# Performance work log

Hardware: AMD Instinct MI355X
Metric: run time of the kernel (lower is better)

Reference implementation:

```python
import jax, jax.numpy as jnp
import numpy as np

N_NODES = 262144
N_EDGES = 4194304
NUM_GRAPHS = 1024
K = 2          # k clusters / particles
D = 4          # particle_latent_dim
D_Q = D // 2   # position part of latent


def setup_inputs() -> dict:
    key = jax.random.key(0)
    ks = jax.random.split(key, 20)
    w = lambda i, shape: 0.1 * jax.random.normal(ks[i], shape, jnp.float32)
    return {
        "x": jax.random.normal(ks[0], (N_NODES, 4), jnp.float32),
        "pos": jax.random.normal(ks[1], (N_NODES, 3), jnp.float32),
        "edge_index": jax.random.randint(ks[2], (2, N_EDGES), 0, N_NODES),
        "batch": jnp.sort(jax.random.randint(ks[3], (N_NODES,), 0, NUM_GRAPHS)),
        "enc_w1": w(4, (9, 16)), "enc_b1": jnp.zeros((16,), jnp.float32),
        "enc_w2": w(5, (16, 16)), "enc_b2": jnp.zeros((16,), jnp.float32),
        "pool_w": w(6, (16, K)), "pool_b": jnp.zeros((K,), jnp.float32),
        "toz_w": w(7, (16, D)), "toz_b": jnp.zeros((D,), jnp.float32),
        "vp_w1": w(8, (1, 32)), "vp_b1": jnp.zeros((32,), jnp.float32),
        "vp_w2": w(9, (32, 1)), "vp_b2": jnp.zeros((1,), jnp.float32),
        "bridge_w": w(10, (K * D, 8 * 4)), "bridge_b": jnp.zeros((8 * 4,), jnp.float32),
    }


def reference(x, pos, edge_index, batch,
              enc_w1, enc_b1, enc_w2, enc_b2,
              pool_w, pool_b, toz_w, toz_b,
              vp_w1, vp_b1, vp_w2, vp_b2,
              bridge_w, bridge_b):
    src = edge_index[0]  # j (source)
    dst = edge_index[1]  # i (target, PyG default flow)

    # --- EquiLayer: edge gather -> small MLP message -> mean scatter ---
    rel_pos = pos[src] - pos[dst]
    dist = jnp.linalg.norm(rel_pos, axis=-1, keepdims=True)       # [E,1]
    feat = jnp.concatenate([x[dst], x[src], dist], axis=-1)       # [E,9]
    msg = jax.nn.silu(feat @ enc_w1 + enc_b1) @ enc_w2 + enc_b2   # [E,16]
    agg = jax.ops.segment_sum(msg, dst, num_segments=N_NODES)     # [N,16]
    cnt = jax.ops.segment_sum(jnp.ones((msg.shape[0], 1), msg.dtype), dst,
                              num_segments=N_NODES)
    h = jax.nn.relu(agg / jnp.maximum(cnt, 1.0))                  # [N,16]

    # --- softmax-weighted scatter pooling over graphs ---
    s = jax.nn.softmax(h @ pool_w + pool_b, axis=-1)              # [N,K]
    weighted = s[:, :, None] * h[:, None, :]                      # [N,K,16]
    pooled = jax.ops.segment_sum(weighted, batch, num_segments=NUM_GRAPHS)  # [B,K,16]
    z = pooled @ toz_w + toz_b                                    # [B,K,D]

    # --- decode ---
    recon = (z.reshape(z.shape[0], -1) @ bridge_w + bridge_b).reshape(-1, 8, 4)

    # --- pairwise potential + forces on position part of latent ---
    iu0, iu1 = np.triu_indices(K, 1)

    def potential(q):
        diff = q[:, :, None, :] - q[:, None, :, :]
        d = jnp.sqrt(jnp.sum(diff * diff, axis=-1) + 1e-6)        # [B,K,K]
        d_flat = d[:, iu0, iu1][..., None]                        # [B,P,1]
        v = jax.nn.softplus(d_flat @ vp_w1 + vp_b1) @ vp_w2 + vp_b2
        return v.sum(axis=1)                                      # [B,1]

    q = z[..., :D_Q]
    V = potential(q)
    forces = -jax.grad(lambda qq: potential(qq).sum())(q)
    return recon, z, s, forces, V
```

## Files before the change

kernel.cpp:

```cpp
#include <hip/hip_runtime.h>
#include <math.h>

#define N_NODES   262144
#define N_EDGES   4194304
#define NUM_GRAPHS 1024
#define NBKT      256
#define BNODE     1024
#define CAPK      17408
#define EPB       8192
#define CSTRIDE   32

typedef _Float16 h8 __attribute__((ext_vector_type(8)));

static __device__ __forceinline__ float fast_rcp(float v) {
    return __builtin_amdgcn_rcpf(v);
}

__global__ __launch_bounds__(512) void bin_pack_kernel(
    const int* __restrict__ ei, const float* __restrict__ x,
    const float* __restrict__ pos,
    int* __restrict__ cursor, int* __restrict__ staged,
    h8* __restrict__ xp)
{
    __shared__ int cnt[NBKT], rcnt[NBKT], lbase[NBKT], gbase[NBKT];
    __shared__ int stage[EPB];
    __shared__ int wsum[4];
    int tid = threadIdx.x;
    if (tid < NBKT) { cnt[tid] = 0; rcnt[tid] = 0; }
    __syncthreads();

    {
        int n0 = blockIdx.x * 512 + tid;
        float4 xv0 = *(const float4*)(x + 4*n0);
        h8 o0;
        o0[0] = (_Float16)xv0.x; o0[1] = (_Float16)xv0.y;
        o0[2] = (_Float16)xv0.z; o0[3] = (_Float16)xv0.w;
        o0[4] = (_Float16)pos[3*n0+0]; o0[5] = (_Float16)pos[3*n0+1];
        o0[6] = (_Float16)pos[3*n0+2]; o0[7] = (_Float16)0.0f;
        xp[n0] = o0;
    }

    int base = blockIdx.x * EPB;
    const int4* d4 = (const int4*)(ei + N_EDGES + base);
    const int4* s4 = (const int4*)(ei + base);
    int4 dv[4];
    #pragma unroll
    for (int i = 0; i < 4; ++i) {
        dv[i] = d4[i*512 + tid];
        atomicAdd(&cnt[dv[i].x >> 10], 1);
        atomicAdd(&cnt[dv[i].y >> 10], 1);
        atomicAdd(&cnt[dv[i].z >> 10], 1);
        atomicAdd(&cnt[dv[i].w >> 10], 1);
    }
    __syncthreads();

    int lane = tid & 63, wid = tid >> 6;
    if (tid < NBKT) {
        int c = cnt[tid];
        int inc = c;
        #pragma unroll
        for (int o = 1; o < 64; o <<= 1) {
            int t = __shfl_up(inc, o);
            if (lane >= o) inc += t;
        }
        if (lane == 63) wsum[wid] = inc;
        cnt[tid] = inc;
    }
    __syncthreads();
    if (tid < NBKT) {
        int inc = cnt[tid];
        int c   = inc;
        int wb = 0;
        #pragma unroll
        for (int w = 0; w < 4; ++w) if (w < wid) wb += wsum[w];
        int prev = __shfl_up(inc, 1);
        int excl = (lane == 0) ? 0 : prev;
        lbase[tid] = wb + excl;
        c = inc - excl;
        gbase[tid] = c ? atomicAdd(cursor + tid*CSTRIDE, c) : 0;
        rcnt[tid] = 0;
    }
    __syncthreads();

    #pragma unroll
    for (int i = 0; i < 4; ++i) {
        int4 sv = s4[i*512 + tid];
        int d, s, bk, r;
        d = dv[i].x; s = sv.x; bk = d >> 10; r = atomicAdd(&rcnt[bk], 1);
        stage[lbase[bk] + r] = ((d & 1023) << 18) | s;
        d = dv[i].y; s = sv.y; bk = d >> 10; r = atomicAdd(&rcnt[bk], 1);
        stage[lbase[bk] + r] = ((d & 1023) << 18) | s;
        d = dv[i].z; s = sv.z; bk = d >> 10; r = atomicAdd(&rcnt[bk], 1);
        stage[lbase[bk] + r] = ((d & 1023) << 18) | s;
        d = dv[i].w; s = sv.w; bk = d >> 10; r = atomicAdd(&rcnt[bk], 1);
        stage[lbase[bk] + r] = ((d & 1023) << 18) | s;
    }
    __syncthreads();

    int sub = tid & 31;
    int grp = tid >> 5;
    #pragma unroll
    for (int pass = 0; pass < NBKT/16; ++pass) {
        int bk  = pass*16 + grp;
        int c2  = rcnt[bk];
        int lb  = lbase[bk];
        int gb  = gbase[bk];
        int lim = CAPK - gb; if (c2 > lim) c2 = lim;
        for (int k = sub; k < c2; k += 32)
            staged[bk*CAPK + gb + k] = stage[lb + k];
    }
}

static __device__ __forceinline__ void edge_contrib(
    const float* __restrict__ sw1, const float* __restrict__ hd,
    float4 xs, float dist, float* __restrict__ acc)
{
    float h[16];
    #pragma unroll
    for (int j4 = 0; j4 < 4; ++j4) {
        float4 w = *(const float4*)&sw1[4*16 + 4*j4];
        h[4*j4+0] = fmaf(xs.x, w.x, hd[4*j4+0]);
        h[4*j4+1] = fmaf(xs.x, w.y, hd[4*j4+1]);
        h[4*j4+2] = fmaf(xs.x, w.z, hd[4*j4+2]);
        h[4*j4+3] = fmaf(xs.x, w.w, hd[4*j4+3]);
    }
    #pragma unroll
    for (int j4 = 0; j4 < 4; ++j4) {
        float4 w = *(const float4*)&sw1[5*16 + 4*j4];
        h[4*j4+0] = fmaf(xs.y, w.x, h[4*j4+0]);
        h[4*j4+1] = fmaf(xs.y, w.y, h[4*j4+1]);
        h[4*j4+2] = fmaf(xs.y, w.z, h[4*j4+2]);
        h[4*j4+3] = fmaf(xs.y, w.w, h[4*j4+3]);
    }
    #pragma unroll
    for (int j4 = 0; j4 < 4; ++j4) {
        float4 w = *(const float4*)&sw1[6*16 + 4*j4];
        h[4*j4+0] = fmaf(xs.z, w.x, h[4*j4+0]);
        h[4*j4+1] = fmaf(xs.z, w.y, h[4*j4+1]);
        h[4*j4+2] = fmaf(xs.z, w.z, h[4*j4+2]);
        h[4*j4+3] = fmaf(xs.z, w.w, h[4*j4+3]);
    }
    #pragma unroll
    for (int j4 = 0; j4 < 4; ++j4) {
        float4 w = *(const float4*)&sw1[7*16 + 4*j4];
        h[4*j4+0] = fmaf(xs.w, w.x, h[4*j4+0]);
        h[4*j4+1] = fmaf(xs.w, w.y, h[4*j4+1]);
        h[4*j4+2] = fmaf(xs.w, w.z, h[4*j4+2]);
        h[4*j4+3] = fmaf(xs.w, w.w, h[4*j4+3]);
    }
    #pragma unroll
    for (int j4 = 0; j4 < 4; ++j4) {
        float4 w = *(const float4*)&sw1[8*16 + 4*j4];
        h[4*j4+0] = fmaf(dist, w.x, h[4*j4+0]);
        h[4*j4+1] = fmaf(dist, w.y, h[4*j4+1]);
        h[4*j4+2] = fmaf(dist, w.z, h[4*j4+2]);
        h[4*j4+3] = fmaf(dist, w.w, h[4*j4+3]);
    }
    #pragma unroll
    for (int j = 0; j < 16; ++j) {
        float sg = fast_rcp(1.0f + __expf(-h[j]));
        acc[j] = fmaf(h[j], sg, acc[j]);
    }
}

__global__ __launch_bounds__(1024, 4) void fused_node_kernel(
    const h8* __restrict__ xp,
    const int* __restrict__ cursor, const int* __restrict__ staged,
    const int* __restrict__ batch,
    const float* __restrict__ w1, const float* __restrict__ b1,
    const float* __restrict__ w2, const float* __restrict__ b2,
    const float* __restrict__ pw, const float* __restrict__ pb,
    float* __restrict__ s_out, float* __restrict__ pooled)
{
    __shared__ int esrc[CAPK];
    __shared__ int ldeg[BNODE];
    __shared__ int wsum[16];
    __shared__ __align__(16) float sw1[144];
    __shared__ float sb1[16];
    __shared__ __align__(16) float sw2[256];
    __shared__ float sb2[16];
    __shared__ float spw[32];
    __shared__ float spb[2];

    int tid = threadIdx.x;
    if (tid < 144) sw1[tid] = w1[tid];
    if (tid >= 144 && tid < 160) sb1[tid - 144] = b1[tid - 144];
    if (tid >= 160 && tid < 176) sb2[tid - 160] = b2[tid - 160];
    if (tid >= 176 && tid < 208) spw[tid - 176] = pw[tid - 176];
    if (tid >= 208 && tid < 210) spb[tid - 208] = pb[tid - 208];
    if (tid >= 256 && tid < 512) sw2[tid - 256] = w2[tid - 256];
    ldeg[tid] = 0;
    __syncthreads();

    int bkt  = blockIdx.x;
    int cnt  = cursor[bkt*CSTRIDE]; if (cnt > CAPK) cnt = CAPK;
    int base = bkt * CAPK;
    int nb0  = bkt * BNODE;

    for (int i = tid; i < cnt; i += 1024)
        atomicAdd(&ldeg[__builtin_nontemporal_load(&staged[base + i]) >> 18], 1);
    __syncthreads();

    int dg   = ldeg[tid];
    int lane = tid & 63, wid = tid >> 6;
    int inc  = dg;
    #pragma unroll
    for (int o = 1; o < 64; o <<= 1) {
        int t = __shfl_up(inc, o);
        if (lane >= o) inc += t;
    }
    if (lane == 63) wsum[wid] = inc;
    __syncthreads();
    int wb = 0;
    #pragma unroll
    for (int w = 0; w < 16; ++w) if (w < wid) wb += wsum[w];
    int r0 = wb + inc - dg;
    ldeg[tid] = r0;
    __syncthreads();

    for (int i = tid; i < cnt; i += 1024) {
        int p  = __builtin_nontemporal_load(&staged[base + i]);
        int lo = p >> 18;
        int r  = atomicAdd(&ldeg[lo], 1);
        esrc[r] = p & 0x3FFFF;
    }
    __syncthreads();

    int n = nb0 + tid;
    h8 rd = xp[n];
    float4 xd = make_float4((float)rd[0], (float)rd[1], (float)rd[2], (float)rd[3]);
    float pdx = (float)rd[4], pdy = (float)rd[5], pdz = (float)rd[6];

    float hd[16];
    #pragma unroll
    for (int j = 0; j < 16; ++j) hd[j] = sb1[j];
    #pragma unroll
    for (int j4 = 0; j4 < 4; ++j4) {
        float4 w0 = *(const float4*)&sw1[0*16 + 4*j4];
        float4 w1r = *(const float4*)&sw1[1*16 + 4*j4];
        float4 w2r = *(const float4*)&sw1[2*16 + 4*j4];
        float4 w3r = *(const float4*)&sw1[3*16 + 4*j4];
        hd[4*j4+0] = fmaf(xd.x, w0.x, hd[4*j4+0]);
        hd[4*j4+1] = fmaf(xd.x, w0.y, hd[4*j4+1]);
        hd[4*j4+2] = fmaf(xd.x, w0.z, hd[4*j4+2]);
        hd[4*j4+3] = fmaf(xd.x, w0.w, hd[4*j4+3]);
        hd[4*j4+0] = fmaf(xd.y, w1r.x, hd[4*j4+0]);
        hd[4*j4+1] = fmaf(xd.y, w1r.y, hd[4*j4+1]);
        hd[4*j4+2] = fmaf(xd.y, w1r.z, hd[4*j4+2]);
        hd[4*j4+3] = fmaf(xd.y, w1r.w, hd[4*j4+3]);
        hd[4*j4+0] = fmaf(xd.z, w2r.x, hd[4*j4+0]);
        hd[4*j4+1] = fmaf(xd.z, w2r.y, hd[4*j4+1]);
        hd[4*j4+2] = fmaf(xd.z, w2r.z, hd[4*j4+2]);
        hd[4*j4+3] = fmaf(xd.z, w2r.w, hd[4*j4+3]);
        hd[4*j4+0] = fmaf(xd.w, w3r.x, hd[4*j4+0]);
        hd[4*j4+1] = fmaf(xd.w, w3r.y, hd[4*j4+1]);
        hd[4*j4+2] = fmaf(xd.w, w3r.z, hd[4*j4+2]);
        hd[4*j4+3] = fmaf(xd.w, w3r.w, hd[4*j4+3]);
    }

    float acc[16];
    #pragma unroll
    for (int j = 0; j < 16; ++j) acc[j] = 0.0f;

    int k = 0;
    for (; k + 2 <= dg; k += 2) {
        int s0 = esrc[r0 + k];
        int s1 = esrc[r0 + k + 1];
        h8 e0 = xp[s0];
        h8 e1 = xp[s1];

        float4 a0 = make_float4((float)e0[0], (float)e0[1], (float)e0[2], (float)e0[3]);
        float dx0 = (float)e0[4] - pdx, dy0 = (float)e0[5] - pdy, dz0 = (float)e0[6] - pdz;
        float dist0 = sqrtf(fmaf(dx0, dx0, fmaf(dy0, dy0, dz0*dz0)));
        edge_contrib(sw1, hd, a0, dist0, acc);

        float4 a1 = make_float4((float)e1[0], (float)e1[1], (float)e1[2], (float)e1[3]);
        float dx1 = (float)e1[4] - pdx, dy1 = (float)e1[5] - pdy, dz1 = (float)e1[6] - pdz;
        float dist1 = sqrtf(fmaf(dx1, dx1, fmaf(dy1, dy1, dz1*dz1)));
        edge_contrib(sw1, hd, a1, dist1, acc);
    }
    if (k < dg) {
        int s0 = esrc[r0 + k];
        h8 e0 = xp[s0];
        float4 a0 = make_float4((float)e0[0], (float)e0[1], (float)e0[2], (float)e0[3]);
        float dx0 = (float)e0[4] - pdx, dy0 = (float)e0[5] - pdy, dz0 = (float)e0[6] - pdz;
        float dist0 = sqrtf(fmaf(dx0, dx0, fmaf(dy0, dy0, dz0*dz0)));
        edge_contrib(sw1, hd, a0, dist0, acc);
    }

    float c = (float)dg;
    float inv = fast_rcp(fmaxf(c, 1.0f));
    float h[16];
    #pragma unroll
    for (int j = 0; j < 16; ++j) h[j] = c * sb2[j];
    #pragma unroll
    for (int i = 0; i < 16; ++i) {
        float f = acc[i];
        #pragma unroll
        for (int j4 = 0; j4 < 4; ++j4) {
            float4 w = *(const float4*)&sw2[i*16 + 4*j4];
            h[4*j4+0] = fmaf(f, w.x, h[4*j4+0]);
            h[4*j4+1] = fmaf(f, w.y, h[4*j4+1]);
            h[4*j4+2] = fmaf(f, w.z, h[4*j4+2]);
            h[4*j4+3] = fmaf(f, w.w, h[4*j4+3]);
        }
    }
    #pragma unroll
    for (int j = 0; j < 16; ++j) h[j] = fmaxf(h[j] * inv, 0.0f);

    float l0 = spb[0], l1 = spb[1];
    #pragma unroll
    for (int j = 0; j < 16; ++j) {
        l0 = fmaf(h[j], spw[2*j+0], l0);
        l1 = fmaf(h[j], spw[2*j+1], l1);
    }
    float m = fmaxf(l0, l1);
    float e0 = __expf(l0 - m), e1 = __expf(l1 - m);
    float r = fast_rcp(e0 + e1);
    float s0 = e0 * r, s1 = e1 * r;
    s_out[2*n+0] = s0;
    s_out[2*n+1] = s1;

    float w[32];
    #pragma unroll
    for (int j = 0; j < 16; ++j) { w[j] = s0 * h[j]; w[16+j] = s1 * h[j]; }

    int b = batch[n];
    #pragma unroll
    for (int o = 1; o < 64; o <<= 1) {
        int bn = __shfl_down(b, o);
        bool take = (lane + o < 64) && (bn == b);
        #pragma unroll
        for (int cc = 0; cc < 32; ++cc) {
            float vn = __shfl_down(w[cc], o);
            if (take) w[cc] += vn;
        }
    }
    int bp = __shfl_up(b, 1);
    if (lane == 0 || bp != b) {
        float* pg = pooled + 32*b;
        #pragma unroll
        for (int cc = 0; cc < 32; ++cc) unsafeAtomicAdd(pg + cc, w[cc]);
    }
}

__global__ __launch_bounds__(256) void graph_kernel(
    const float* __restrict__ pooled,
    const float* __restrict__ toz_w, const float* __restrict__ toz_b,
    const float* __restrict__ vp_w1, const float* __restrict__ vp_b1,
    const float* __restrict__ vp_w2, const float* __restrict__ vp_b2,
    const float* __restrict__ bridge_w, const float* __restrict__ bridge_b,
    float* __restrict__ out_recon, float* __restrict__ out_z,
    float* __restrict__ out_forces, float* __restrict__ out_V)
{
    int g = blockIdx.x * 256 + threadIdx.x;
    if (g >= NUM_GRAPHS) return;

    const float* P = pooled + 32*g;
    float z[8];
    #pragma unroll
    for (int k = 0; k < 2; ++k) {
        #pragma unroll
        for (int d = 0; d < 4; ++d) {
            float a = toz_b[d];
            #pragma unroll
            for (int i = 0; i < 16; ++i) a = fmaf(P[16*k+i], toz_w[4*i+d], a);
            z[4*k+d] = a;
        }
    }
    #pragma unroll
    for (int i = 0; i < 8; ++i) out_z[8*g+i] = z[i];

    #pragma unroll
    for (int j = 0; j < 32; ++j) {
        float a = bridge_b[j];
        #pragma unroll
        for (int i = 0; i < 8; ++i) a = fmaf(z[i], bridge_w[32*i+j], a);
        out_recon[32*g+j] = a;
    }

    float d0 = z[0]-z[4], d1 = z[1]-z[5];
    float dd = sqrtf(d0*d0 + d1*d1 + 1e-6f);

    float V = vp_b2[0];
    float dV = 0.0f;
    #pragma unroll
    for (int j = 0; j < 32; ++j) {
        float w1 = vp_w1[j];
        float t  = fmaf(dd, w1, vp_b1[j]);
        float et = __expf(t);
        float sp = __logf(1.0f + et);
        float sg = et / (1.0f + et);
        float w2 = vp_w2[j];
        V  = fmaf(sp, w2, V);
        dV = fmaf(sg * w1, w2, dV);
    }
    out_V[g] = V;

    float scale = dV / dd;
    float gx = scale * d0, gy = scale * d1;
    out_forces[4*g+0] = -gx;
    out_forces[4*g+1] = -gy;
    out_forces[4*g+2] =  gx;
    out_forces[4*g+3] =  gy;
}

extern "C" void kernel_launch(void* const* d_in, const int* in_sizes, int n_in,
                              void* d_out, int out_size, void* d_ws, size_t ws_size,
                              hipStream_t stream) {
    const float* x        = (const float*)d_in[0];
    const float* pos      = (const float*)d_in[1];
    const int*   ei       = (const int*)  d_in[2];
    const int*   batch    = (const int*)  d_in[3];
    const float* enc_w1   = (const float*)d_in[4];
    const float* enc_b1   = (const float*)d_in[5];
    const float* enc_w2   = (const float*)d_in[6];
    const float* enc_b2   = (const float*)d_in[7];
    const float* pool_w   = (const float*)d_in[8];
    const float* pool_b   = (const float*)d_in[9];
    const float* toz_w    = (const float*)d_in[10];
    const float* toz_b    = (const float*)d_in[11];
    const float* vp_w1    = (const float*)d_in[12];
    const float* vp_b1    = (const float*)d_in[13];
    const float* vp_w2    = (const float*)d_in[14];
    const float* vp_b2    = (const float*)d_in[15];
    const float* bridge_w = (const float*)d_in[16];
    const float* bridge_b = (const float*)d_in[17];

    int*   cursor = (int*)d_ws;
    float* pooled = (float*)d_ws + NBKT*CSTRIDE;
    int*   staged = (int*)d_ws + NBKT*CSTRIDE + 32768;
    h8*    xp     = (h8*)(staged + (size_t)NBKT*CAPK);

    float* out        = (float*)d_out;
    float* out_recon  = out;
    float* out_z      = out_recon + 1024*32;
    float* out_s      = out_z + 1024*8;
    float* out_forces = out_s + (size_t)N_NODES*2;
    float* out_V      = out_forces + 1024*4;

    hipMemsetAsync(d_ws, 0, (size_t)(NBKT*CSTRIDE + 32768) * sizeof(float), stream);

    bin_pack_kernel<<<N_EDGES/EPB, 512, 0, stream>>>(ei, x, pos, cursor, staged, xp);
    fused_node_kernel<<<NBKT, 1024, 0, stream>>>(
        xp, cursor, staged, batch,
        enc_w1, enc_b1, enc_w2, enc_b2, pool_w, pool_b, out_s, pooled);
    graph_kernel<<<NUM_GRAPHS/256, 256, 0, stream>>>(
        pooled, toz_w, toz_b, vp_w1, vp_b1, vp_w2, vp_b2,
        bridge_w, bridge_b, out_recon, out_z, out_forces, out_V);
}
```

Before: 212.3 us.

## Replace atomic global cursors with fixed per-block segments and drop memset

The edge binning stage now writes each (bucket, block) pair into a fixed-capacity segment with a per-segment count, so it no longer needs global atomic cursor allocation. Blocks grow to 1024 threads handling 16384 edges each, and zeroing of the pooled buffer moves into the bin kernel, which removes the hipMemsetAsync launch. The node kernel walks 256 segments per bucket wave by wave instead of one contiguous range. The cost is more scattered, partly empty segment reads, and a risk of silently truncating edges when a segment exceeds 112 entries (the expected count is 64).

```diff
diff --git a/kernel.cpp b/kernel.cpp
--- a/kernel.cpp
+++ b/kernel.cpp
@@ -7,8 +7,9 @@
 #define NBKT      256
 #define BNODE     1024
 #define CAPK      17408
-#define EPB       8192
-#define CSTRIDE   32
+#define NBLK      256
+#define EPB       16384
+#define SEGCAP    112
 
 typedef _Float16 h8 __attribute__((ext_vector_type(8)));
 
@@ -16,28 +17,29 @@
     return __builtin_amdgcn_rcpf(v);
 }
 
-__global__ __launch_bounds__(512) void bin_pack_kernel(
+__global__ __launch_bounds__(1024) void bin_pack_kernel(
     const int* __restrict__ ei, const float* __restrict__ x,
     const float* __restrict__ pos,
-    int* __restrict__ cursor, int* __restrict__ staged,
-    h8* __restrict__ xp)
+    int* __restrict__ cnts, int* __restrict__ staged,
+    h8* __restrict__ xp, float* __restrict__ pooled)
 {
-    __shared__ int cnt[NBKT], rcnt[NBKT], lbase[NBKT], gbase[NBKT];
+    __shared__ int cnt[NBKT], rcnt[NBKT], lbase[NBKT];
+    __shared__ int wsum[4];
     __shared__ int stage[EPB];
-    __shared__ int wsum[4];
     int tid = threadIdx.x;
     if (tid < NBKT) { cnt[tid] = 0; rcnt[tid] = 0; }
     __syncthreads();
 
     {
-        int n0 = blockIdx.x * 512 + tid;
-        float4 xv0 = *(const float4*)(x + 4*n0);
-        h8 o0;
-        o0[0] = (_Float16)xv0.x; o0[1] = (_Float16)xv0.y;
-        o0[2] = (_Float16)xv0.z; o0[3] = (_Float16)xv0.w;
-        o0[4] = (_Float16)pos[3*n0+0]; o0[5] = (_Float16)pos[3*n0+1];
-        o0[6] = (_Float16)pos[3*n0+2]; o0[7] = (_Float16)0.0f;
-        xp[n0] = o0;
+        int n0 = blockIdx.x * 1024 + tid;
+        float4 xv = *(const float4*)(x + 4*n0);
+        h8 o;
+        o[0] = (_Float16)xv.x; o[1] = (_Float16)xv.y;
+        o[2] = (_Float16)xv.z; o[3] = (_Float16)xv.w;
+        o[4] = (_Float16)pos[3*n0+0]; o[5] = (_Float16)pos[3*n0+1];
+        o[6] = (_Float16)pos[3*n0+2]; o[7] = (_Float16)0.0f;
+        xp[n0] = o;
+        if (blockIdx.x < 32) pooled[blockIdx.x*1024 + tid] = 0.0f;
     }
 
     int base = blockIdx.x * EPB;
@@ -46,7 +48,7 @@
     int4 dv[4];
     #pragma unroll
     for (int i = 0; i < 4; ++i) {
-        dv[i] = d4[i*512 + tid];
+        dv[i] = d4[i*1024 + tid];
         atomicAdd(&cnt[dv[i].x >> 10], 1);
         atomicAdd(&cnt[dv[i].y >> 10], 1);
         atomicAdd(&cnt[dv[i].z >> 10], 1);
@@ -56,8 +58,7 @@
 
     int lane = tid & 63, wid = tid >> 6;
     if (tid < NBKT) {
-        int c = cnt[tid];
-        int inc = c;
+        int inc = cnt[tid];
         #pragma unroll
         for (int o = 1; o < 64; o <<= 1) {
             int t = __shfl_up(inc, o);
@@ -68,23 +69,19 @@
     }
     __syncthreads();
     if (tid < NBKT) {
-        int inc = cnt[tid];
-        int c   = inc;
-        int wb = 0;
-        #pragma unroll
-        for (int w = 0; w < 4; ++w) if (w < wid) wb += wsum[w];
+        int inc  = cnt[tid];
         int prev = __shfl_up(inc, 1);
         int excl = (lane == 0) ? 0 : prev;
+        int wb = 0;
+        #pragma unroll
+        for (int w = 0; w < 4; ++w) if (w < wid) wb += wsum[w];
         lbase[tid] = wb + excl;
-        c = inc - excl;
-        gbase[tid] = c ? atomicAdd(cursor + tid*CSTRIDE, c) : 0;
-        rcnt[tid] = 0;
     }
     __syncthreads();
 
     #pragma unroll
     for (int i = 0; i < 4; ++i) {
-        int4 sv = s4[i*512 + tid];
+        int4 sv = s4[i*1024 + tid];
         int d, s, bk, r;
         d = dv[i].x; s = sv.x; bk = d >> 10; r = atomicAdd(&rcnt[bk], 1);
         stage[lbase[bk] + r] = ((d & 1023) << 18) | s;
@@ -97,17 +94,17 @@
     }
     __syncthreads();
 
-    int sub = tid & 31;
-    int grp = tid >> 5;
-    #pragma unroll
-    for (int pass = 0; pass < NBKT/16; ++pass) {
-        int bk  = pass*16 + grp;
+    int sub = tid & 31, grp = tid >> 5;
+    #pragma unroll
+    for (int pass = 0; pass < NBKT/32; ++pass) {
+        int bk  = pass*32 + grp;
         int c2  = rcnt[bk];
         int lb  = lbase[bk];
-        int gb  = gbase[bk];
-        int lim = CAPK - gb; if (c2 > lim) c2 = lim;
+        if (c2 > SEGCAP) c2 = SEGCAP;
+        size_t sb = ((size_t)bk*NBLK + blockIdx.x)*SEGCAP;
         for (int k = sub; k < c2; k += 32)
-            staged[bk*CAPK + gb + k] = stage[lb + k];
+            staged[sb + k] = stage[lb + k];
+        if (sub == 0) cnts[bk*NBLK + blockIdx.x] = c2;
     }
 }
 
@@ -165,7 +162,7 @@
 
 __global__ __launch_bounds__(1024, 4) void fused_node_kernel(
     const h8* __restrict__ xp,
-    const int* __restrict__ cursor, const int* __restrict__ staged,
+    const int* __restrict__ cnts, const int* __restrict__ staged,
     const int* __restrict__ batch,
     const float* __restrict__ w1, const float* __restrict__ b1,
     const float* __restrict__ w2, const float* __restrict__ b2,
@@ -174,6 +171,7 @@
 {
     __shared__ int esrc[CAPK];
     __shared__ int ldeg[BNODE];
+    __shared__ int scnt[NBLK];
     __shared__ int wsum[16];
     __shared__ __align__(16) float sw1[144];
     __shared__ float sb1[16];
@@ -183,27 +181,30 @@
     __shared__ float spb[2];
 
     int tid = threadIdx.x;
+    int bkt = blockIdx.x;
     if (tid < 144) sw1[tid] = w1[tid];
     if (tid >= 144 && tid < 160) sb1[tid - 144] = b1[tid - 144];
     if (tid >= 160 && tid < 176) sb2[tid - 160] = b2[tid - 160];
     if (tid >= 176 && tid < 208) spw[tid - 176] = pw[tid - 176];
     if (tid >= 208 && tid < 210) spb[tid - 208] = pb[tid - 208];
     if (tid >= 256 && tid < 512) sw2[tid - 256] = w2[tid - 256];
+    if (tid >= 512 && tid < 768) scnt[tid - 512] = cnts[bkt*NBLK + (tid - 512)];
     ldeg[tid] = 0;
     __syncthreads();
 
-    int bkt  = blockIdx.x;
-    int cnt  = cursor[bkt*CSTRIDE]; if (cnt > CAPK) cnt = CAPK;
-    int base = bkt * CAPK;
+    int lane = tid & 63, wid = tid >> 6;
     int nb0  = bkt * BNODE;
 
-    for (int i = tid; i < cnt; i += 1024)
-        atomicAdd(&ldeg[__builtin_nontemporal_load(&staged[base + i]) >> 18], 1);
-    __syncthreads();
-
-    int dg   = ldeg[tid];
-    int lane = tid & 63, wid = tid >> 6;
-    int inc  = dg;
+    for (int s = wid; s < NBLK; s += 16) {
+        int c = scnt[s];
+        const int* seg = staged + ((size_t)bkt*NBLK + s)*SEGCAP;
+        for (int i = lane; i < c; i += 64)
+            atomicAdd(&ldeg[seg[i] >> 18], 1);
+    }
+    __syncthreads();
+
+    int dg  = ldeg[tid];
+    int inc = dg;
     #pragma unroll
     for (int o = 1; o < 64; o <<= 1) {
         int t = __shfl_up(inc, o);
@@ -218,11 +219,14 @@
     ldeg[tid] = r0;
     __syncthreads();
 
-    for (int i = tid; i < cnt; i += 1024) {
-        int p  = __builtin_nontemporal_load(&staged[base + i]);
-        int lo = p >> 18;
-        int r  = atomicAdd(&ldeg[lo], 1);
-        esrc[r] = p & 0x3FFFF;
+    for (int s = wid; s < NBLK; s += 16) {
+        int c = scnt[s];
+        const int* seg = staged + ((size_t)bkt*NBLK + s)*SEGCAP;
+        for (int i = lane; i < c; i += 64) {
+            int p = seg[i];
+            int r = atomicAdd(&ldeg[p >> 18], 1);
+            if (r < CAPK) esrc[r] = p & 0x3FFFF;
+        }
     }
     __syncthreads();
 
@@ -427,10 +431,10 @@
     const float* bridge_w = (const float*)d_in[16];
     const float* bridge_b = (const float*)d_in[17];
 
-    int*   cursor = (int*)d_ws;
-    float* pooled = (float*)d_ws + NBKT*CSTRIDE;
-    int*   staged = (int*)d_ws + NBKT*CSTRIDE + 32768;
-    h8*    xp     = (h8*)(staged + (size_t)NBKT*CAPK);
+    int*   cnts   = (int*)d_ws;
+    float* pooled = (float*)d_ws + NBKT*NBLK;
+    int*   staged = (int*)d_ws + NBKT*NBLK + 32768;
+    h8*    xp     = (h8*)(staged + (size_t)NBKT*NBLK*SEGCAP);
 
     float* out        = (float*)d_out;
     float* out_recon  = out;
@@ -439,11 +443,9 @@
     float* out_forces = out_s + (size_t)N_NODES*2;
     float* out_V      = out_forces + 1024*4;
 
-    hipMemsetAsync(d_ws, 0, (size_t)(NBKT*CSTRIDE + 32768) * sizeof(float), stream);
-
-    bin_pack_kernel<<<N_EDGES/EPB, 512, 0, stream>>>(ei, x, pos, cursor, staged, xp);
+    bin_pack_kernel<<<NBLK, 1024, 0, stream>>>(ei, x, pos, cnts, staged, xp, pooled);
     fused_node_kernel<<<NBKT, 1024, 0, stream>>>(
-        xp, cursor, staged, batch,
+        xp, cnts, staged, batch,
         enc_w1, enc_b1, enc_w2, enc_b2, pool_w, pool_b, out_s, pooled);
     graph_kernel<<<NUM_GRAPHS/256, 256, 0, stream>>>(
         pooled, toz_w, toz_b, vp_w1, vp_b1, vp_w2, vp_b2,
```

After: 212.1 us. No clear change (-0.1%).
